# Performance work log

Measured on AMD Instinct MI355X. Metric: run time of the kernel, lower is better.

Reference implementation:

```python
import jax, jax.numpy as jnp
import numpy as np

NEG_SLOPE = 0.2  # PyG GATConv default negative_slope
HEADS1, HID = 8, 256


def gat_conv(x, src, dst, W, att_src, att_dst, bias, heads, out_ch):
    """PyG-style GATConv: project, per-edge attention, segment softmax over dst, scatter-add."""
    N = x.shape[0]
    h = (x @ W.T).reshape(N, heads, out_ch)                 # [N,H,C]
    a_s = jnp.einsum('nhc,hc->nh', h, att_src)              # [N,H]
    a_d = jnp.einsum('nhc,hc->nh', h, att_dst)
    e = jax.nn.leaky_relu(a_s[src] + a_d[dst], NEG_SLOPE)   # [E,H]
    m = jax.ops.segment_max(e, dst, num_segments=N)         # stable softmax per dst node
    ex = jnp.exp(e - m[dst])
    denom = jax.ops.segment_sum(ex, dst, num_segments=N)
    alpha = ex / (denom[dst] + 1e-16)                       # [E,H]
    out = jax.ops.segment_sum(alpha[:, :, None] * h[src], dst, num_segments=N)  # [N,H,C]
    return out.reshape(N, heads * out_ch) + bias


def setup_inputs() -> dict:
    key = jax.random.key(0)
    ks = jax.random.split(key, 20)
    Nc, Ncol, E = 4000, 16000, 100000
    nf, cf, gain, hid, H, emb = 64, 128, 2, HID, HEADS1, 128
    s = 0.05
    return {
        'constraints_state': jax.random.normal(ks[0], (Nc, nf), jnp.float32),
        'columns_state':     jax.random.normal(ks[1], (Ncol, cf), jnp.float32),
        'edges':             jax.random.randint(ks[2], (2, E), 0, Nc + Ncol, jnp.int64),
        'W_node': jax.random.normal(ks[3], (hid, nf * gain), jnp.float32) * s,
        'b_node': jnp.zeros((hid,), jnp.float32),
        'W_col':  jax.random.normal(ks[4], (hid, cf * gain), jnp.float32) * s,
        'b_col':  jnp.zeros((hid,), jnp.float32),
        'W1':       jax.random.normal(ks[5], (H * hid, hid), jnp.float32) * s,
        'att_src1': jax.random.normal(ks[6], (H, hid), jnp.float32) * s,
        'att_dst1': jax.random.normal(ks[7], (H, hid), jnp.float32) * s,
        'b1':       jnp.zeros((H * hid,), jnp.float32),
        'W2':       jax.random.normal(ks[8], (hid, H * hid), jnp.float32) * s,
        'att_src2': jax.random.normal(ks[9], (1, hid), jnp.float32) * s,
        'att_dst2': jax.random.normal(ks[10], (1, hid), jnp.float32) * s,
        'b2':       jnp.zeros((hid,), jnp.float32),
        'W_out': jax.random.normal(ks[11], (emb, hid), jnp.float32) * s,
        'b_out': jnp.zeros((emb,), jnp.float32),
    }


def reference(constraints_state, columns_state, edges,
              W_node, b_node, W_col, b_col,
              W1, att_src1, att_dst1, b1,
              W2, att_src2, att_dst2, b2,
              W_out, b_out):
    gain = 2
    x_n = jnp.tile(constraints_state, (1, gain))
    x_c = jnp.tile(columns_state, (1, gain))
    h_n = jax.nn.relu(x_n @ W_node.T + b_node)
    h_c = jax.nn.relu(x_c @ W_col.T + b_col)
    x = jnp.concatenate([h_n, h_c], axis=0)                 # [N, hid]
    N = x.shape[0]
    loops = jnp.arange(N)
    # conv1: edges as given (+ self-loops, PyG default)
    src1 = jnp.concatenate([edges[0], loops])
    dst1 = jnp.concatenate([edges[1], loops])
    x = jax.nn.relu(gat_conv(x, src1, dst1, W1, att_src1, att_dst1, b1, HEADS1, HID))
    # conv2: flipped edges (+ self-loops), 1 head
    src2 = jnp.concatenate([edges[1], loops])
    dst2 = jnp.concatenate([edges[0], loops])
    x = jax.nn.relu(gat_conv(x, src2, dst2, W2, att_src2, att_dst2, b2, 1, HID))
    logits = x[-columns_state.shape[0]:] @ W_out.T + b_out  # [Ncol, embed_dim]
    return logits
```

## Files before the change

kernel.cpp:

```cpp
#include <hip/hip_runtime.h>


#define NEG_SLOPE 0.2f

typedef __attribute__((ext_vector_type(8))) short bf16x8;
typedef __attribute__((ext_vector_type(4))) float f32x4;

__device__ __forceinline__ float bf2f(unsigned short u) {
  return __uint_as_float(((unsigned)u) << 16);
}
__device__ __forceinline__ unsigned short f2bf(float f) {
  unsigned u = __float_as_uint(f);
  u += 0x7fffu + ((u >> 16) & 1u);
  return (unsigned short)(u >> 16);
}

__device__ __forceinline__ void async_copy16(const void* g, void* l) {
  __builtin_amdgcn_global_load_lds(
      (const __attribute__((address_space(1))) unsigned int*)g,
      (__attribute__((address_space(3))) unsigned int*)l, 16, 0, 0);
}

__global__ void prep(const float* __restrict__ Wn, const float* __restrict__ Wc,
                     const float* __restrict__ W1, const float* __restrict__ W2,
                     const float* __restrict__ Wout,
                     const float* __restrict__ cons, const float* __restrict__ cols,
                     const float* __restrict__ att_s1, const float* __restrict__ att_d1,
                     unsigned short* __restrict__ Wn_b, unsigned short* __restrict__ Wc_b,
                     unsigned short* __restrict__ W1b, unsigned short* __restrict__ W2b,
                     unsigned short* __restrict__ Woutb,
                     unsigned short* __restrict__ consb, unsigned short* __restrict__ colsb,
                     float* __restrict__ v_s1, float* __restrict__ v_d1,
                     int n_cons, int n_cols) {
  const int S0 = 256 * 64;
  const int S1 = 256 * 128;
  const int S2 = 2048 * 256;
  const int S3 = 256 * 2048;
  const int S4 = 128 * 256;
  const int S5 = 2048;
  int total = S0 + S1 + S2 + S3 + S4 + n_cons + n_cols + S5;
  for (int idx = blockIdx.x * 256 + threadIdx.x; idx < total; idx += gridDim.x * 256) {
    int i = idx;
    if (i < S0) { int o = i >> 6, j = i & 63;
      Wn_b[i] = f2bf(Wn[o * 128 + j] + Wn[o * 128 + 64 + j]); continue; }
    i -= S0;
    if (i < S1) { int o = i >> 7, j = i & 127;
      Wc_b[i] = f2bf(Wc[o * 256 + j] + Wc[o * 256 + 128 + j]); continue; }
    i -= S1;
    if (i < S2) { W1b[i] = f2bf(W1[i]); continue; }
    i -= S2;
    if (i < S3) { W2b[i] = f2bf(W2[i]); continue; }
    i -= S3;
    if (i < S4) { Woutb[i] = f2bf(Wout[i]); continue; }
    i -= S4;
    if (i < n_cons) { consb[i] = f2bf(cons[i]); continue; }
    i -= n_cons;
    if (i < n_cols) { colsb[i] = f2bf(cols[i]); continue; }
    i -= n_cols;
    {
      int h = i >> 8, k = i & 255;
      const float* Wrow = W1 + (size_t)h * 256 * 256 + k;
      const float* as = att_s1 + h * 256;
      const float* ad = att_d1 + h * 256;
      float s = 0.f, d = 0.f;
      for (int c = 0; c < 256; ++c) {
        float w = Wrow[(size_t)c * 256];
        s += as[c] * w;
        d += ad[c] * w;
      }
      v_s1[i] = s; v_d1[i] = d;
    }
  }
}

__global__ __launch_bounds__(256) void a1_dots(const unsigned short* __restrict__ xb,
                                               const float* __restrict__ v_s,
                                               const float* __restrict__ v_d,
                                               float* __restrict__ a_s,
                                               float* __restrict__ a_d, int N) {
  __shared__ float vs[2048], vd[2048];
  for (int i = threadIdx.x; i < 2048; i += 256) { vs[i] = v_s[i]; vd[i] = v_d[i]; }
  __syncthreads();
  int n = blockIdx.x * 256 + threadIdx.x;
  if (n >= N) return;
  const unsigned short* row = xb + (size_t)n * 256;
  float s[8] = {}, d[8] = {};
  for (int c = 0; c < 256; c += 8) {
    bf16x8 xv = *(const bf16x8*)(row + c);
    float xf[8];
#pragma unroll
    for (int i = 0; i < 8; ++i) xf[i] = bf2f(((const unsigned short*)&xv)[i]);
#pragma unroll
    for (int h = 0; h < 8; ++h)
#pragma unroll
      for (int i = 0; i < 8; ++i) {
        s[h] += xf[i] * vs[h * 256 + c + i];
        d[h] += xf[i] * vd[h * 256 + c + i];
      }
  }
#pragma unroll
  for (int h = 0; h < 8; ++h) { a_s[n * 8 + h] = s[h]; a_d[n * 8 + h] = d[h]; }
}

template <bool C_BF16, bool BIAS, bool RELU, bool BDIAG>
__global__ __launch_bounds__(512) void gemm_mfma_bt(const unsigned short* __restrict__ A,
                                                    const unsigned short* __restrict__ W,
                                                    const float* __restrict__ bias,
                                                    void* __restrict__ Cv,
                                                    int M, int K, int Nout, int lda) {
  __shared__ short smem[2 * 128 * 64];
  short* sA = smem;
  short* sB = smem + 128 * 64;
  float* Cf = (float*)Cv;
  unsigned short* Cb = (unsigned short*)Cv;

  const int tid = threadIdx.x;
  const int lane = tid & 63, w = tid >> 6;
  const int m0 = blockIdx.y * 128, n0 = blockIdx.x * 128;
  const int koff = BDIAG ? (n0 >> 8) << 8 : 0;
  const int wm = (w & 3) * 32, wn = (w >> 2) * 64;
  const int fr = lane & 15;
  const int frs = fr & 7;
  const int quad = lane >> 4;

  f32x4 acc[2][4];
#pragma unroll
  for (int i = 0; i < 2; ++i)
#pragma unroll
    for (int j = 0; j < 4; ++j) acc[i][j] = (f32x4){0.f, 0.f, 0.f, 0.f};

  for (int k0 = 0; k0 < K; k0 += 64) {
#pragma unroll
    for (int i = 0; i < 2; ++i) {
      int c = i * 512 + tid;
      int row = c >> 3, kc = c & 7;
      int kcs = kc ^ (row & 7);
      int grow = m0 + row;
      if (grow >= M) grow = M - 1;
      async_copy16(A + (size_t)grow * lda + koff + k0 + kcs * 8, &sA[(i * 512 + w * 64) * 8]);
    }
#pragma unroll
    for (int i = 0; i < 2; ++i) {
      int c = i * 512 + tid;
      int row = c >> 3, kc = c & 7;
      int kcs = kc ^ (row & 7);
      async_copy16(W + (size_t)(n0 + row) * K + k0 + kcs * 8, &sB[(i * 512 + w * 64) * 8]);
    }
    __syncthreads();

#pragma unroll
    for (int ks = 0; ks < 2; ++ks) {
      bf16x8 af[2], bfr[4];
#pragma unroll
      for (int mi = 0; mi < 2; ++mi) {
        int row = wm + mi * 16 + fr;
        af[mi] = *(const bf16x8*)&sA[(row * 8 + ((ks * 4 + quad) ^ frs)) * 8];
      }
#pragma unroll
      for (int ni = 0; ni < 4; ++ni) {
        int row = wn + ni * 16 + fr;
        bfr[ni] = *(const bf16x8*)&sB[(row * 8 + ((ks * 4 + quad) ^ frs)) * 8];
      }
#pragma unroll
      for (int mi = 0; mi < 2; ++mi)
#pragma unroll
        for (int ni = 0; ni < 4; ++ni)
          acc[mi][ni] = __builtin_amdgcn_mfma_f32_16x16x32_bf16(
              af[mi], bfr[ni], acc[mi][ni], 0, 0, 0);
    }
    __syncthreads();
  }

  if (C_BF16) {
    unsigned short* hsh = (unsigned short*)smem;
#pragma unroll
    for (int mi = 0; mi < 2; ++mi)
#pragma unroll
      for (int ni = 0; ni < 4; ++ni) {
        int col = wn + ni * 16 + fr;
        float bv = BIAS ? bias[n0 + col] : 0.f;
        f32x4 v = acc[mi][ni];
#pragma unroll
        for (int r = 0; r < 4; ++r) {
          int row = wm + mi * 16 + quad * 4 + r;
          float x = v[r] + bv;
          if (RELU) x = fmaxf(x, 0.f);
          hsh[row * 128 + (col ^ (((row >> 2) & 3) << 5))] = f2bf(x);
        }
      }
    __syncthreads();
#pragma unroll
    for (int i = 0; i < 4; ++i) {
      int slot = i * 512 + tid;
      int row = slot >> 4, cg = slot & 15;
      int colbase = cg * 8;
      bf16x8 val = *(const bf16x8*)&hsh[row * 128 + (colbase ^ (((row >> 2) & 3) << 5))];
      int grow = m0 + row;
      if (grow < M)
        *(bf16x8*)(Cb + (size_t)grow * Nout + n0 + colbase) = val;
    }
  } else {
#pragma unroll
    for (int mi = 0; mi < 2; ++mi)
#pragma unroll
      for (int ni = 0; ni < 4; ++ni) {
        int col = n0 + wn + ni * 16 + fr;
        float bv = BIAS ? bias[col] : 0.f;
        f32x4 v = acc[mi][ni];
#pragma unroll
        for (int r = 0; r < 4; ++r) {
          int row = m0 + wm + mi * 16 + quad * 4 + r;
          if (row < M) {
            float x = v[r] + bv;
            if (RELU) x = fmaxf(x, 0.f);
            Cf[(size_t)row * Nout + col] = x;
          }
        }
      }
  }
}

__global__ __launch_bounds__(512) void gemm_mfma_k2048(const unsigned short* __restrict__ A,
                                                       const unsigned short* __restrict__ W,
                                                       unsigned short* __restrict__ C,
                                                       const float* __restrict__ att_s,
                                                       const float* __restrict__ att_d,
                                                       float* __restrict__ a_s,
                                                       float* __restrict__ a_d,
                                                       int M, int K) {
  __shared__ short sA[32 * 64];
  __shared__ short sB[256 * 64];
  const int tid = threadIdx.x;
  const int lane = tid & 63, w = tid >> 6;
  const int m0 = blockIdx.x * 32;
  const int fr = lane & 15, quad = lane >> 4;
  const int frs = fr & 7;

  f32x4 acc[2][2];
#pragma unroll
  for (int i = 0; i < 2; ++i)
#pragma unroll
    for (int j = 0; j < 2; ++j) acc[i][j] = (f32x4){0.f, 0.f, 0.f, 0.f};

  for (int k0 = 0; k0 < K; k0 += 64) {
    if (w < 4) {
      int row = tid >> 3, kc = tid & 7;
      int kcs = kc ^ (row & 7);
      int grow = m0 + row;
      if (grow >= M) grow = M - 1;
      async_copy16(A + (size_t)grow * K + k0 + kcs * 8, &sA[(w * 64) * 8]);
    }
#pragma unroll
    for (int i = 0; i < 4; ++i) {
      int c = i * 512 + tid;
      int row = c >> 3, kc = c & 7;
      int kcs = kc ^ (row & 7);
      async_copy16(W + (size_t)row * K + k0 + kcs * 8, &sB[(i * 512 + w * 64) * 8]);
    }
    __syncthreads();

#pragma unroll
    for (int ks = 0; ks < 2; ++ks) {
      bf16x8 af[2], bfr[2];
#pragma unroll
      for (int mi = 0; mi < 2; ++mi) {
        int row = mi * 16 + fr;
        af[mi] = *(const bf16x8*)&sA[(row * 8 + ((ks * 4 + quad) ^ frs)) * 8];
      }
#pragma unroll
      for (int ni = 0; ni < 2; ++ni) {
        int row = w * 32 + ni * 16 + fr;
        bfr[ni] = *(const bf16x8*)&sB[(row * 8 + ((ks * 4 + quad) ^ frs)) * 8];
      }
#pragma unroll
      for (int mi = 0; mi < 2; ++mi)
#pragma unroll
        for (int ni = 0; ni < 2; ++ni)
          acc[mi][ni] = __builtin_amdgcn_mfma_f32_16x16x32_bf16(
              af[mi], bfr[ni], acc[mi][ni], 0, 0, 0);
    }
    __syncthreads();
  }

  unsigned short* hsh = (unsigned short*)sB;
#pragma unroll
  for (int mi = 0; mi < 2; ++mi)
#pragma unroll
    for (int ni = 0; ni < 2; ++ni) {
      int col = w * 32 + ni * 16 + fr;
      f32x4 v = acc[mi][ni];
#pragma unroll
      for (int r = 0; r < 4; ++r) {
        int rl = mi * 16 + quad * 4 + r;
        hsh[rl * 256 + col] = f2bf(v[r]);
      }
    }
  __syncthreads();

#pragma unroll
  for (int i = 0; i < 2; ++i) {
    int slot = i * 512 + tid;
    int row = slot >> 5, cg = slot & 31;
    int grow = m0 + row;
    if (grow < M)
      *(bf16x8*)(C + (size_t)grow * 256 + cg * 8) = *(const bf16x8*)&hsh[row * 256 + cg * 8];
  }

  int r = tid >> 4;
  int cbase = (tid & 15) * 16;
  float s = 0.f, d = 0.f;
#pragma unroll
  for (int q = 0; q < 2; ++q) {
    bf16x8 hv8 = *(const bf16x8*)&hsh[r * 256 + cbase + q * 8];
    const unsigned short* hp = (const unsigned short*)&hv8;
#pragma unroll
    for (int i = 0; i < 8; ++i) {
      int c = cbase + q * 8 + i;
      float hv = bf2f(hp[i]);
      s += hv * att_s[c];
      d += hv * att_d[c];
    }
  }
#pragma unroll
  for (int off = 8; off; off >>= 1) {
    s += __shfl_down(s, off);
    d += __shfl_down(d, off);
  }
  if ((tid & 15) == 0 && m0 + r < M) {
    a_s[m0 + r] = s;
    a_d[m0 + r] = d;
  }
}

__global__ void build_count(const void* __restrict__ edges_raw, int E, int N,
                            int* __restrict__ esrc, int* __restrict__ edst,
                            int* __restrict__ cnt1, int* __restrict__ cnt2, int E1) {
  const long long* p64 = (const long long*)edges_raw;
  const int* p32 = (const int*)edges_raw;
  bool is64 = true;
#pragma unroll
  for (int i = 0; i < 8; ++i) {
    long long v = p64[i];
    if (v < 0 || v >= N) is64 = false;
  }
  int idx = blockIdx.x * 256 + threadIdx.x;
  if (idx >= E1) return;
  int s, d;
  if (idx < E) {
    if (is64) { s = (int)p64[idx]; d = (int)p64[E + idx]; }
    else      { s = p32[idx];      d = p32[E + idx]; }
  } else {
    s = d = idx - E;
  }
  esrc[idx] = s;
  edst[idx] = d;
  atomicAdd(&cnt1[d], 1);
  atomicAdd(&cnt2[s], 1);
}

__device__ __forceinline__ void scan_one(const int* __restrict__ cnt,
                                         int* __restrict__ indptr,
                                         int* __restrict__ cur, int N, int* buf) {
  int t = threadIdx.x, lane = t & 63, w = t >> 6;
  int running = 0;
  for (int base = 0; base < N; base += 1024) {
    int v = (base + t < N) ? cnt[base + t] : 0;
    int incl = v;
#pragma unroll
    for (int off = 1; off < 64; off <<= 1) {
      int y = __shfl_up(incl, off);
      if (lane >= off) incl += y;
    }
    if (lane == 63) buf[w] = incl;
    __syncthreads();
    if (t < 16) {
      int x = buf[t];
#pragma unroll
      for (int off = 1; off < 16; off <<= 1) {
        int y = __shfl_up(x, off);
        if (t >= off) x += y;
      }
      buf[t] = x;
    }
    __syncthreads();
    int woff = w ? buf[w - 1] : 0;
    int tot = buf[15];
    if (base + t < N) {
      int excl = running + woff + incl - v;
      indptr[base + t] = excl;
      cur[base + t] = excl;
    }
    running += tot;
    __syncthreads();
  }
  if (t == 0) indptr[N] = running;
  __syncthreads();
}

__global__ __launch_bounds__(1024) void scan2_kernel(const int* cnt1, int* indptr1, int* cur1,
                                                     const int* cnt2, int* indptr2, int* cur2,
                                                     int N) {
  __shared__ int buf[16];
  scan_one(cnt1, indptr1, cur1, N, buf);
  scan_one(cnt2, indptr2, cur2, N, buf);
}

__global__ void scatter_edges(const int* __restrict__ esrc, const int* __restrict__ edst,
                              int* __restrict__ cur1, int* __restrict__ cur2,
                              int* __restrict__ nbr1, int* __restrict__ nbr2, int E1) {
  int e = blockIdx.x * 256 + threadIdx.x;
  if (e >= E1) return;
  int s = esrc[e], d = edst[e];
  int p1 = atomicAdd(&cur1[d], 1);
  nbr1[p1] = s;
  int p2 = atomicAdd(&cur2[s], 1);
  nbr2[p2] = d;
}

__global__ __launch_bounds__(256) void alpha1_kernel(const float* __restrict__ a_s,
                                                     const float* __restrict__ a_d,
                                                     const int* __restrict__ indptr,
                                                     const int* __restrict__ nbr,
                                                     float* __restrict__ alpha, int N) {
  int n = blockIdx.x * 256 + threadIdx.x;
  if (n >= N) return;
  int start = indptr[n], end = indptr[n + 1];
  float ad[8];
  *(float4*)&ad[0] = *(const float4*)&a_d[n * 8];
  *(float4*)&ad[4] = *(const float4*)&a_d[n * 8 + 4];
  float m[8], ssum[8];
#pragma unroll
  for (int h = 0; h < 8; ++h) { m[h] = -1e30f; ssum[h] = 0.f; }
  for (int p = start; p < end; ++p) {
    int s = nbr[p];
    float as[8];
    *(float4*)&as[0] = *(const float4*)&a_s[s * 8];
    *(float4*)&as[4] = *(const float4*)&a_s[s * 8 + 4];
#pragma unroll
    for (int h = 0; h < 8; ++h) {
      float e = as[h] + ad[h];
      e = e > 0.f ? e : NEG_SLOPE * e;
      float nm = fmaxf(m[h], e);
      ssum[h] = ssum[h] * __expf(m[h] - nm) + __expf(e - nm);
      m[h] = nm;
    }
  }
  float inv[8];
#pragma unroll
  for (int h = 0; h < 8; ++h) inv[h] = 1.f / (ssum[h] + 1e-16f);
  for (int p = start; p < end; ++p) {
    int s = nbr[p];
    float as[8];
    *(float4*)&as[0] = *(const float4*)&a_s[s * 8];
    *(float4*)&as[4] = *(const float4*)&a_s[s * 8 + 4];
    float av[8];
#pragma unroll
    for (int h = 0; h < 8; ++h) {
      float e = as[h] + ad[h];
      e = e > 0.f ? e : NEG_SLOPE * e;
      av[h] = __expf(e - m[h]) * inv[h];
    }
    *(float4*)&alpha[(size_t)p * 8] = *(const float4*)&av[0];
    *(float4*)&alpha[(size_t)p * 8 + 4] = *(const float4*)&av[4];
  }
}

__global__ __launch_bounds__(256) void agg1_kernel(const unsigned short* __restrict__ xb,
                                                   const float* __restrict__ alpha,
                                                   const int* __restrict__ indptr,
                                                   const int* __restrict__ nbr,
                                                   unsigned short* __restrict__ agg,
                                                   int N) {
  __shared__ float al_sh[4][64 * 8];
  const int w = threadIdx.x >> 6, lane = threadIdx.x & 63;
  const int dst = blockIdx.x * 4 + w;
  if (dst >= N) return;
  const int start = indptr[dst];
  const int deg = indptr[dst + 1] - start;
  const int c0 = lane * 4;

  float acc[8][4];
#pragma unroll
  for (int h = 0; h < 8; ++h)
#pragma unroll
    for (int i = 0; i < 4; ++i) acc[h][i] = 0.f;

  for (int base = 0; base < deg; base += 64) {
    int cnt = min(64, deg - base);
    int s = 0;
    if (lane < cnt) {
      int slot = start + base + lane;
      s = nbr[slot];
      f32x4 a0 = *(const f32x4*)&alpha[(size_t)slot * 8];
      f32x4 a1 = *(const f32x4*)&alpha[(size_t)slot * 8 + 4];
      *(f32x4*)&al_sh[w][lane * 8] = a0;
      *(f32x4*)&al_sh[w][lane * 8 + 4] = a1;
    }
    __builtin_amdgcn_wave_barrier();
    for (int j = 0; j < cnt; ++j) {
      int sj = __shfl(s, j);
      f32x4 alo = *(const f32x4*)&al_sh[w][j * 8];
      f32x4 ahi = *(const f32x4*)&al_sh[w][j * 8 + 4];
      ushort4 xv = *(const ushort4*)(xb + (size_t)sj * 256 + c0);
      float x0 = bf2f(xv.x), x1 = bf2f(xv.y), x2 = bf2f(xv.z), x3 = bf2f(xv.w);
#pragma unroll
      for (int h = 0; h < 4; ++h) {
        acc[h][0] += alo[h] * x0; acc[h][1] += alo[h] * x1;
        acc[h][2] += alo[h] * x2; acc[h][3] += alo[h] * x3;
      }
#pragma unroll
      for (int h = 0; h < 4; ++h) {
        acc[h + 4][0] += ahi[h] * x0; acc[h + 4][1] += ahi[h] * x1;
        acc[h + 4][2] += ahi[h] * x2; acc[h + 4][3] += ahi[h] * x3;
      }
    }
    __builtin_amdgcn_wave_barrier();
  }

  unsigned short* op = agg + (size_t)dst * 2048;
#pragma unroll
  for (int h = 0; h < 8; ++h) {
    unsigned short ov[4];
#pragma unroll
    for (int i = 0; i < 4; ++i) ov[i] = f2bf(acc[h][i]);
    *((ushort4*)(op + h * 256 + c0)) = *((const ushort4*)ov);
  }
}

__global__ __launch_bounds__(256) void agg2_fused(const unsigned short* __restrict__ h2,
                                                  const float* __restrict__ a_s,
                                                  const float* __restrict__ a_d,
                                                  const int* __restrict__ indptr,
                                                  const int* __restrict__ nbr,
                                                  const float* __restrict__ b2,
                                                  unsigned short* __restrict__ x3,
                                                  int Nc, int Ncol) {
  const int w = threadIdx.x >> 6, lane = threadIdx.x & 63;
  const int i0 = blockIdx.x * 4 + w;
  if (i0 >= Ncol) return;
  const int dst = Nc + i0;
  const int start = indptr[dst];
  const int deg = indptr[dst + 1] - start;
  const float ad = a_d[dst];
  float run_m = -1e30f, run_s = 0.f;
  float acc[4] = {0.f, 0.f, 0.f, 0.f};
  const int c0 = lane * 4;

  for (int base = 0; base < deg; base += 64) {
    int cnt = min(64, deg - base);
    float ev = -1e30f;
    int s = 0;
    if (lane < cnt) {
      s = nbr[start + base + lane];
      float e = a_s[s] + ad;
      ev = e > 0.f ? e : NEG_SLOPE * e;
    }
    float cm = ev;
#pragma unroll
    for (int off = 32; off; off >>= 1) cm = fmaxf(cm, __shfl_xor(cm, off));
    float nm = fmaxf(run_m, cm);
    float sc = __expf(run_m - nm);
    float e = (lane < cnt) ? __expf(ev - nm) : 0.f;
    float cs = e;
#pragma unroll
    for (int off = 32; off; off >>= 1) cs += __shfl_xor(cs, off);
    run_s = run_s * sc + cs;
    run_m = nm;
#pragma unroll
    for (int i = 0; i < 4; ++i) acc[i] *= sc;
    for (int j = 0; j < cnt; ++j) {
      int sj = __shfl(s, j);
      float al = __shfl(e, j);
      ushort4 hv = *(const ushort4*)(h2 + (size_t)sj * 256 + c0);
      acc[0] += al * bf2f(hv.x);
      acc[1] += al * bf2f(hv.y);
      acc[2] += al * bf2f(hv.z);
      acc[3] += al * bf2f(hv.w);
    }
  }

  float inv = 1.f / (run_s + 1e-16f);
  float4 bv = *(const float4*)&b2[c0];
  unsigned short ov[4];
  ov[0] = f2bf(fmaxf(acc[0] * inv + bv.x, 0.f));
  ov[1] = f2bf(fmaxf(acc[1] * inv + bv.y, 0.f));
  ov[2] = f2bf(fmaxf(acc[2] * inv + bv.z, 0.f));
  ov[3] = f2bf(fmaxf(acc[3] * inv + bv.w, 0.f));
  *((ushort4*)(x3 + (size_t)i0 * 256 + c0)) = *((const ushort4*)ov);
}

extern "C" void kernel_launch(void* const* d_in, const int* in_sizes, int n_in,
                              void* d_out, int out_size, void* d_ws, size_t ws_size,
                              hipStream_t stream) {
  (void)n_in; (void)out_size; (void)ws_size;
  const float* constraints = (const float*)d_in[0];
  const float* columns     = (const float*)d_in[1];
  const void*  edges       = d_in[2];
  const float* W_node = (const float*)d_in[3];
  const float* b_node = (const float*)d_in[4];
  const float* W_col  = (const float*)d_in[5];
  const float* b_col  = (const float*)d_in[6];
  const float* W1       = (const float*)d_in[7];
  const float* att_src1 = (const float*)d_in[8];
  const float* att_dst1 = (const float*)d_in[9];
  const float* b1       = (const float*)d_in[10];
  const float* W2       = (const float*)d_in[11];
  const float* att_src2 = (const float*)d_in[12];
  const float* att_dst2 = (const float*)d_in[13];
  const float* b2       = (const float*)d_in[14];
  const float* W_out    = (const float*)d_in[15];
  const float* b_out    = (const float*)d_in[16];

  const int Nc   = in_sizes[0] / 64;
  const int Ncol = in_sizes[1] / 128;
  const int E    = in_sizes[2] / 2;
  const int N    = Nc + Ncol;
  const int E1   = E + N;

  char* p = (char*)d_ws;
  size_t off = 0;
  auto alloc = [&](size_t nbytes) -> void* {
    void* r = p + off;
    off = (off + nbytes + 255) & ~(size_t)255;
    return r;
  };
  unsigned short* Wn_b  = (unsigned short*)alloc(2ull * 256 * 64);
  unsigned short* Wc_b  = (unsigned short*)alloc(2ull * 256 * 128);
  unsigned short* W1b   = (unsigned short*)alloc(2ull * 2048 * 256);
  unsigned short* W2b   = (unsigned short*)alloc(2ull * 256 * 2048);
  unsigned short* Woutb = (unsigned short*)alloc(2ull * 128 * 256);
  unsigned short* consb = (unsigned short*)alloc(2ull * (size_t)Nc * 64);
  unsigned short* colsb = (unsigned short*)alloc(2ull * (size_t)Ncol * 128);
  unsigned short* xb    = (unsigned short*)alloc(2ull * (size_t)N * 256);
  float* v_s1 = (float*)alloc(sizeof(float) * 8 * 256);
  float* v_d1 = (float*)alloc(sizeof(float) * 8 * 256);
  float* a_s1 = (float*)alloc(sizeof(float) * (size_t)N * 8);
  float* a_d1 = (float*)alloc(sizeof(float) * (size_t)N * 8);
  int* esrc = (int*)alloc(4ull * E1);
  int* edst = (int*)alloc(4ull * E1);
  int* cnt1 = (int*)alloc(4ull * 2 * N);
  int* cnt2 = cnt1 + N;
  int* indptr1 = (int*)alloc(4ull * (N + 1));
  int* cur1    = (int*)alloc(4ull * N);
  int* indptr2 = (int*)alloc(4ull * (N + 1));
  int* cur2    = (int*)alloc(4ull * N);
  int* nbr1 = (int*)alloc(4ull * E1);
  int* nbr2 = (int*)alloc(4ull * E1);
  float* alpha1 = (float*)alloc(sizeof(float) * 8ull * E1);
  unsigned short* agg = (unsigned short*)alloc(2ull * (size_t)N * 2048);
  unsigned short* x2  = (unsigned short*)alloc(2ull * (size_t)N * 2048);
  unsigned short* h2b = (unsigned short*)alloc(2ull * (size_t)N * 256);
  float* a_s2 = (float*)alloc(sizeof(float) * (size_t)N);
  float* a_d2 = (float*)alloc(sizeof(float) * (size_t)N);
  unsigned short* x3 = (unsigned short*)alloc(2ull * (size_t)Ncol * 256);

  hipMemsetAsync(cnt1, 0, 4ull * 2 * N, stream);
  prep<<<1024, 256, 0, stream>>>(W_node, W_col, W1, W2, W_out, constraints, columns,
                                 att_src1, att_dst1,
                                 Wn_b, Wc_b, W1b, W2b, Woutb, consb, colsb,
                                 v_s1, v_d1, Nc * 64, Ncol * 128);

  gemm_mfma_bt<true, true, true, false><<<dim3(2, (Nc + 127) / 128), 512, 0, stream>>>(
      consb, Wn_b, b_node, xb, Nc, 64, 256, 64);
  gemm_mfma_bt<true, true, true, false><<<dim3(2, (Ncol + 127) / 128), 512, 0, stream>>>(
      colsb, Wc_b, b_col, xb + (size_t)Nc * 256, Ncol, 128, 256, 128);

  a1_dots<<<(N + 255) / 256, 256, 0, stream>>>(xb, v_s1, v_d1, a_s1, a_d1, N);

  build_count<<<(E1 + 255) / 256, 256, 0, stream>>>(edges, E, N, esrc, edst, cnt1, cnt2, E1);
  scan2_kernel<<<1, 1024, 0, stream>>>(cnt1, indptr1, cur1, cnt2, indptr2, cur2, N);
  scatter_edges<<<(E1 + 255) / 256, 256, 0, stream>>>(esrc, edst, cur1, cur2, nbr1, nbr2, E1);

  alpha1_kernel<<<(N + 255) / 256, 256, 0, stream>>>(a_s1, a_d1, indptr1, nbr1, alpha1, N);
  agg1_kernel<<<(N + 3) / 4, 256, 0, stream>>>(xb, alpha1, indptr1, nbr1, agg, N);
  gemm_mfma_bt<true, true, true, true><<<dim3(16, (N + 127) / 128), 512, 0, stream>>>(
      agg, W1b, b1, x2, N, 256, 2048, 2048);

  gemm_mfma_k2048<<<(N + 31) / 32, 512, 0, stream>>>(
      x2, W2b, h2b, att_src2, att_dst2, a_s2, a_d2, N, 2048);
  agg2_fused<<<(Ncol + 3) / 4, 256, 0, stream>>>(h2b, a_s2, a_d2, indptr2, nbr2, b2, x3,
                                                 Nc, Ncol);

  gemm_mfma_bt<false, true, false, false><<<dim3(1, (Ncol + 127) / 128), 512, 0, stream>>>(
      x3, Woutb, b_out, (float*)d_out, Ncol, 256, 128, 256);
}
```

Before: 370.4 us.

## Load GEMM fragments directly from global into registers with double buffering

Drops the LDS staging of A and W tiles in the K=2048 conv2 projection GEMM. Each wave now loads its MFMA fragments straight from global memory into registers, using a two-stage register double buffer to overlap loads with MFMAs, and the loop no longer needs __syncthreads. LDS shrinks to just the epilogue buffer and launch bounds now request 4 blocks per CU for higher occupancy. The cost is that W rows are fetched separately by every block without LDS sharing, which relies on L2/cache hits, and register pressure rises from the fragment buffers.

```diff
diff --git a/kernel.cpp b/kernel.cpp
--- a/kernel.cpp
+++ b/kernel.cpp
@@ -220,21 +220,27 @@
   }
 }
 
-__global__ __launch_bounds__(512) void gemm_mfma_k2048(const unsigned short* __restrict__ A,
-                                                       const unsigned short* __restrict__ W,
-                                                       unsigned short* __restrict__ C,
-                                                       const float* __restrict__ att_s,
-                                                       const float* __restrict__ att_d,
-                                                       float* __restrict__ a_s,
-                                                       float* __restrict__ a_d,
-                                                       int M, int K) {
-  __shared__ short sA[32 * 64];
-  __shared__ short sB[256 * 64];
+__global__ __launch_bounds__(512, 4) void gemm_mfma_k2048(
+    const unsigned short* __restrict__ A,
+    const unsigned short* __restrict__ W,
+    unsigned short* __restrict__ C,
+    const float* __restrict__ att_s,
+    const float* __restrict__ att_d,
+    float* __restrict__ a_s,
+    float* __restrict__ a_d,
+    int M, int K) {
+  __shared__ short hsh_s[32 * 256];
   const int tid = threadIdx.x;
   const int lane = tid & 63, w = tid >> 6;
   const int m0 = blockIdx.x * 32;
   const int fr = lane & 15, quad = lane >> 4;
-  const int frs = fr & 7;
+
+  int ra0 = m0 + fr;       if (ra0 >= M) ra0 = M - 1;
+  int ra1 = m0 + 16 + fr;  if (ra1 >= M) ra1 = M - 1;
+  const unsigned short* pa0 = A + (size_t)ra0 * K + quad * 8;
+  const unsigned short* pa1 = A + (size_t)ra1 * K + quad * 8;
+  const unsigned short* pb0 = W + (size_t)(w * 32 + fr) * K + quad * 8;
+  const unsigned short* pb1 = W + (size_t)(w * 32 + 16 + fr) * K + quad * 8;
 
   f32x4 acc[2][2];
 #pragma unroll
@@ -242,47 +248,44 @@
 #pragma unroll
     for (int j = 0; j < 2; ++j) acc[i][j] = (f32x4){0.f, 0.f, 0.f, 0.f};
 
-  for (int k0 = 0; k0 < K; k0 += 64) {
-    if (w < 4) {
-      int row = tid >> 3, kc = tid & 7;
-      int kcs = kc ^ (row & 7);
-      int grow = m0 + row;
-      if (grow >= M) grow = M - 1;
-      async_copy16(A + (size_t)grow * K + k0 + kcs * 8, &sA[(w * 64) * 8]);
-    }
-#pragma unroll
-    for (int i = 0; i < 4; ++i) {
-      int c = i * 512 + tid;
-      int row = c >> 3, kc = c & 7;
-      int kcs = kc ^ (row & 7);
-      async_copy16(W + (size_t)row * K + k0 + kcs * 8, &sB[(i * 512 + w * 64) * 8]);
-    }
-    __syncthreads();
-
-#pragma unroll
-    for (int ks = 0; ks < 2; ++ks) {
-      bf16x8 af[2], bfr[2];
-#pragma unroll
-      for (int mi = 0; mi < 2; ++mi) {
-        int row = mi * 16 + fr;
-        af[mi] = *(const bf16x8*)&sA[(row * 8 + ((ks * 4 + quad) ^ frs)) * 8];
-      }
-#pragma unroll
-      for (int ni = 0; ni < 2; ++ni) {
-        int row = w * 32 + ni * 16 + fr;
-        bfr[ni] = *(const bf16x8*)&sB[(row * 8 + ((ks * 4 + quad) ^ frs)) * 8];
-      }
-#pragma unroll
-      for (int mi = 0; mi < 2; ++mi)
-#pragma unroll
-        for (int ni = 0; ni < 2; ++ni)
-          acc[mi][ni] = __builtin_amdgcn_mfma_f32_16x16x32_bf16(
-              af[mi], bfr[ni], acc[mi][ni], 0, 0, 0);
-    }
-    __syncthreads();
-  }
-
-  unsigned short* hsh = (unsigned short*)sB;
+  bf16x8 A0[4], B0[4], A1[4], B1[4];
+
+  auto LDA = [&](bf16x8* d, int k) {
+    d[0] = *(const bf16x8*)(pa0 + k);
+    d[1] = *(const bf16x8*)(pa1 + k);
+    d[2] = *(const bf16x8*)(pa0 + k + 32);
+    d[3] = *(const bf16x8*)(pa1 + k + 32);
+  };
+  auto LDB = [&](bf16x8* d, int k) {
+    d[0] = *(const bf16x8*)(pb0 + k);
+    d[1] = *(const bf16x8*)(pb1 + k);
+    d[2] = *(const bf16x8*)(pb0 + k + 32);
+    d[3] = *(const bf16x8*)(pb1 + k + 32);
+  };
+
+#define MM_K64(Af, Bf)                                                       \
+  {                                                                          \
+    _Pragma("unroll") for (int ks = 0; ks < 2; ++ks)                         \
+        _Pragma("unroll") for (int mi = 0; mi < 2; ++mi)                     \
+            _Pragma("unroll") for (int ni = 0; ni < 2; ++ni)                 \
+                acc[mi][ni] = __builtin_amdgcn_mfma_f32_16x16x32_bf16(       \
+                    (Af)[ks * 2 + mi], (Bf)[ks * 2 + ni], acc[mi][ni], 0, 0, 0); \
+  }
+
+  LDA(A0, 0); LDB(B0, 0);
+  int k0 = 0;
+  for (; k0 + 128 < K; k0 += 128) {
+    LDA(A1, k0 + 64);  LDB(B1, k0 + 64);
+    MM_K64(A0, B0);
+    LDA(A0, k0 + 128); LDB(B0, k0 + 128);
+    MM_K64(A1, B1);
+  }
+  LDA(A1, k0 + 64); LDB(B1, k0 + 64);
+  MM_K64(A0, B0);
+  MM_K64(A1, B1);
+#undef MM_K64
+
+  unsigned short* hsh = (unsigned short*)hsh_s;
 #pragma unroll
   for (int mi = 0; mi < 2; ++mi)
 #pragma unroll
```

Result: slower. 493.6 us (+33.3%).
